# Performance work log

Measured on AMD Instinct MI355X. Metric: run time of the kernel, lower is better.

The kernel has to match this reference:

```python
import jax, jax.numpy as jnp
import numpy as np

N_NODES = 10000

def rgcn_layer(x, edge_index, basis, comp, root, bias):
    # x: [N, Fin]; edge_index: [R, 2, E] int; basis: [B, Fin, Fout]; comp: [R, B]
    R, _, E = edge_index.shape
    N = x.shape[0]
    src = edge_index[:, 0]  # [R, E]
    dst = edge_index[:, 1]  # [R, E]
    # basis-decomposed per-relation weights: W_r = sum_b comp[r,b] * basis[b]
    W = jnp.einsum('rb,bio->rio', comp, basis)          # [R, Fin, Fout]
    x_src = x[src]                                       # [R, E, Fin] gather
    msg = jnp.einsum('rei,rio->reo', x_src, W)           # [R, E, Fout]
    # per-relation mean aggregation onto destination nodes
    seg = (jnp.arange(R, dtype=dst.dtype)[:, None] * N + dst).reshape(-1)  # [R*E]
    agg = jax.ops.segment_sum(msg.reshape(R * E, -1), seg, num_segments=R * N)
    deg = jax.ops.segment_sum(jnp.ones((R * E,), x.dtype), seg, num_segments=R * N)
    agg = agg / jnp.maximum(deg, 1.0)[:, None]
    agg = agg.reshape(R, N, -1).sum(0)                   # sum over relations
    return agg + x @ root + bias


def setup_inputs() -> dict:
    key = jax.random.key(0)
    ks = jax.random.split(key, 10)
    s = 0.05  # scale params for numerical sanity
    return {
        'x_drug': jax.random.normal(ks[0], (N_NODES, 2048), jnp.float32),
        'drug_w': jax.random.normal(ks[1], (2048, 128), jnp.float32) * s,
        'edge_index': jax.random.randint(ks[2], (100, 2, 5000), 0, N_NODES, jnp.int32),
        'basis1': jax.random.normal(ks[3], (8, 128, 64), jnp.float32) * s,
        'comp1': jax.random.normal(ks[4], (100, 8), jnp.float32) * s,
        'root1': jax.random.normal(ks[5], (128, 64), jnp.float32) * s,
        'bias1': jnp.zeros((64,), jnp.float32),
        'basis2': jax.random.normal(ks[6], (8, 64, 20), jnp.float32) * s,
        'comp2': jax.random.normal(ks[7], (100, 8), jnp.float32) * s,
        'root2': jax.random.normal(ks[8], (64, 20), jnp.float32) * s,
        'bias2': jnp.zeros((20,), jnp.float32),
    }


def reference(x_drug, drug_w, edge_index, basis1, comp1, root1, bias1,
              basis2, comp2, root2, bias2):
    x = x_drug @ drug_w                                   # dense projection [N, 128]
    h = rgcn_layer(x, edge_index, basis1, comp1, root1, bias1)   # [N, 64]
    h = jax.nn.relu(h)
    out = rgcn_layer(h, edge_index, basis2, comp2, root2, bias2)  # [N, 20]
    return out
```

## Files before the change

kernel.cpp:

```cpp
#include <hip/hip_runtime.h>

#define NN 10000
#define RR 100
#define EE 5000
#define D0 2048
#define D1 128
#define D2 64
#define D3 20
#define NE (RR*EE)
#define MAXD 128

using short8  = __attribute__((ext_vector_type(8))) short;
using float4e = __attribute__((ext_vector_type(4))) float;

typedef const __attribute__((address_space(1))) void g_void;
typedef __attribute__((address_space(3))) void l_void;

__device__ __forceinline__ unsigned short f2bf(float f) {
  unsigned int u = __float_as_uint(f);
  unsigned int r = u + 0x7fffu + ((u >> 16) & 1u);
  return (unsigned short)(r >> 16);
}
__device__ __forceinline__ float bf2f(unsigned short u) {
  return __uint_as_float(((unsigned int)u) << 16);
}
__device__ __forceinline__ unsigned int pk2(float lo, float hi) {
  return ((unsigned int)f2bf(hi) << 16) | (unsigned int)f2bf(lo);
}

#define CURB 10
#define WTBLK 1024
#define W1BLK 288
#define W2BLK 72
__global__ __launch_bounds__(256) void prep_kernel(
    const float* __restrict__ W, const float* __restrict__ root1,
    const float* __restrict__ basis1, const float* __restrict__ root2,
    const float* __restrict__ basis2, int4* __restrict__ cur4,
    unsigned short* __restrict__ Btw, unsigned short* __restrict__ Wc1T,
    unsigned short* __restrict__ Wc2T) {
  const int b = blockIdx.x, tid = threadIdx.x;
  if (b < CURB) {
    int i = b * 256 + tid;
    if (i < 2504) cur4[i] = make_int4(0, 0, 0, 0);
  } else if (b < CURB + WTBLK) {
    int idx = (b - CURB) * 256 + tid;
    int n = idx >> 11, k = idx & 2047;
    Btw[idx] = f2bf(W[(size_t)k * 128 + n]);
  } else if (b < CURB + WTBLK + W1BLK) {
    int idx = (b - CURB - WTBLK) * 256 + tid;
    int o = idx / 1152, j = idx - o * 1152;
    float v = (j < 128) ? root1[j * 64 + o] : basis1[(j - 128) * 64 + o];
    Wc1T[idx] = f2bf(v);
  } else {
    int idx = (b - CURB - WTBLK - W1BLK) * 256 + tid;
    int c = idx / 576, j = idx - c * 576;
    float v = 0.f;
    if (c < 20) v = (j < 64) ? root2[j * 20 + c] : basis2[(j - 64) * 20 + c];
    Wc2T[idx] = f2bf(v);
  }
}

__global__ void scatter_kernel(const int* __restrict__ ei,
                               int* __restrict__ cur, int* __restrict__ rec) {
  int gid = blockIdx.x * 256 + threadIdx.x;
  if (gid >= NE) return;
  int r = gid / EE, e = gid - r * EE;
  int s = ei[r * 2 * EE + e];
  int d = ei[r * 2 * EE + EE + e];
  int p = atomicAdd(&cur[d], 1);
  if (p < MAXD) rec[d * MAXD + p] = (r << 14) | s;
}

__global__ __launch_bounds__(256) void finalize_kernel(
    const int* __restrict__ cur, const int* __restrict__ rec,
    float* __restrict__ esc) {
  __shared__ int hist[4][RR];
  const int tid = threadIdx.x;
  const int wv = tid >> 6, lane = tid & 63;
  const int n = blockIdx.x * 4 + wv;
  for (int i = lane; i < RR; i += 64) hist[wv][i] = 0;
  __syncthreads();
  int cnt = cur[n]; if (cnt > MAXD) cnt = MAXD;
  int r0 = 0, r1 = 0;
  if (lane < cnt) {
    r0 = rec[n * MAXD + lane] >> 14;
    atomicAdd(&hist[wv][r0], 1);
  }
  if (lane + 64 < cnt) {
    r1 = rec[n * MAXD + lane + 64] >> 14;
    atomicAdd(&hist[wv][r1], 1);
  }
  __syncthreads();
  if (lane < cnt)      esc[n * MAXD + lane]      = 1.0f / (float)hist[wv][r0];
  if (lane + 64 < cnt) esc[n * MAXD + lane + 64] = 1.0f / (float)hist[wv][r1];
}

__global__ __launch_bounds__(256) void gemm0_mfma(
    const float* __restrict__ A, const unsigned short* __restrict__ Btw,
    unsigned short* __restrict__ xb) {
  __shared__ __align__(16) unsigned short Asb[2][16 * 64];
  __shared__ __align__(16) unsigned short Bsb[2][128 * 64];
  const int tid = threadIdx.x;
  const int m0 = blockIdx.x * 16;
  const int wv = tid >> 6, lane = tid & 63;
  const int lrow = lane & 15, quad = lane >> 4;

  const int ar = tid >> 4, ag = tid & 15;
  const float* Ap = &A[(size_t)(m0 + ar) * D0 + ag * 4];
  const int aw = (ar * 128 + ((ag * 8) ^ ((ar & 7) << 4))) >> 1;

  const int rowB = wv * 32 + (lane >> 3);
  const int gch  = (lane & 7) ^ (lane >> 3);
  const unsigned short* BgBase = &Btw[(size_t)rowB * D0 + gch * 8];
  const int ldsB = wv * 2048;

  float4 a0;

#define G0_LOADB(buf, c)                                                     \
  { _Pragma("unroll")                                                        \
    for (int i = 0; i < 4; i++) {                                            \
      __builtin_amdgcn_global_load_lds(                                      \
          (g_void*)(BgBase + (size_t)i * 8 * D0 + (c) * 64),                 \
          (l_void*)&Bsb[buf][ldsB + i * 512], 16, 0, 0);                     \
    } }

#define G0_LOADA(c)  { a0 = *(const float4*)(Ap + (c) * 64); }

#define G0_STOREA(buf)                                                  \
  { uint2 p0;                                                           \
    p0.x = pk2(a0.x, a0.y); p0.y = pk2(a0.z, a0.w);                     \
    *(uint2*)&Asb[buf][aw] = p0; }

#define G0_COMPUTE(buf)                                                 \
  { const int aswz = (lrow & 7) << 4;                                   \
    _Pragma("unroll")                                                   \
    for (int kk = 0; kk < 2; kk++) {                                    \
      short8 af = *(const short8*)&Asb[buf][(lrow * 128 + ((quad * 16 + kk * 64) ^ aswz)) >> 1]; \
      _Pragma("unroll")                                                 \
      for (int nt = 0; nt < 2; nt++) {                                  \
        const int brow = wv * 32 + nt * 16 + lrow;                      \
        short8 bfr = *(const short8*)&Bsb[buf][(brow * 128 + ((quad * 16 + kk * 64) ^ ((brow & 7) << 4))) >> 1]; \
        acc[nt] = __builtin_amdgcn_mfma_f32_16x16x32_bf16(af, bfr, acc[nt], 0, 0, 0); \
      }                                                                 \
    } }

  float4e acc[2];
#pragma unroll
  for (int i = 0; i < 2; i++) { acc[i][0]=0.f; acc[i][1]=0.f; acc[i][2]=0.f; acc[i][3]=0.f; }

  G0_LOADB(0, 0);
  G0_LOADA(0);
  G0_STOREA(0);
  __syncthreads();

#pragma unroll 4
  for (int c = 0; c < 32; c++) {
    if (c < 31) {
      G0_LOADB((c + 1) & 1, c + 1);
      G0_LOADA(c + 1);
      __builtin_amdgcn_sched_barrier(0);
    }
    G0_COMPUTE(c & 1);
    if (c < 31) G0_STOREA((c + 1) & 1);
    __syncthreads();
  }

#pragma unroll
  for (int nt = 0; nt < 2; nt++) {
    const int col = wv * 32 + nt * 16 + lrow;
#pragma unroll
    for (int r = 0; r < 4; r++) {
      const int row = m0 + quad * 4 + r;
      xb[(size_t)row * D1 + col] = f2bf(acc[nt][r]);
    }
  }
}

__global__ __launch_bounds__(256) void agg1e_kernel(
    const unsigned short* __restrict__ xb, const int* __restrict__ cur,
    const int* __restrict__ rec, const float* __restrict__ esc,
    const float* __restrict__ comp, unsigned short* __restrict__ A1b) {
  __shared__ float s_comp[RR * 8];
  const int tid = threadIdx.x;
  for (int i = tid; i < RR * 8; i += 256) s_comp[i] = comp[i];
  __syncthreads();
  const int wv = tid >> 6, lane = tid & 63;
  const int n = blockIdx.x * 4 + wv;
  if (n >= NN) return;
  float acc[8][2];
#pragma unroll
  for (int b = 0; b < 8; b++) { acc[b][0] = 0.f; acc[b][1] = 0.f; }
  int cnt = cur[n]; if (cnt > MAXD) cnt = MAXD;
  const int beg = n * MAXD, end = beg + cnt;
  int idx = beg;
  for (; idx + 3 < end; idx += 4) {
    int rc[4]; float sc[4]; unsigned int xv[4];
#pragma unroll
    for (int u = 0; u < 4; u++) {
      rc[u] = rec[idx + u];
      sc[u] = esc[idx + u];
    }
#pragma unroll
    for (int u = 0; u < 4; u++)
      xv[u] = *(const unsigned int*)&xb[(size_t)(rc[u] & 16383) * D1 + lane * 2];
#pragma unroll
    for (int u = 0; u < 4; u++) {
      const float* cb = &s_comp[(rc[u] >> 14) * 8];
      float x0 = __uint_as_float((xv[u] & 0xffffu) << 16);
      float x1 = __uint_as_float(xv[u] & 0xffff0000u);
#pragma unroll
      for (int b = 0; b < 8; b++) {
        float w = sc[u] * cb[b];
        acc[b][0] += w * x0;
        acc[b][1] += w * x1;
      }
    }
  }
  for (; idx < end; idx++) {
    int rc = rec[idx];
    float sc = esc[idx];
    unsigned int xv = *(const unsigned int*)&xb[(size_t)(rc & 16383) * D1 + lane * 2];
    const float* cb = &s_comp[(rc >> 14) * 8];
    float x0 = __uint_as_float((xv & 0xffffu) << 16);
    float x1 = __uint_as_float(xv & 0xffff0000u);
#pragma unroll
    for (int b = 0; b < 8; b++) {
      float w = sc * cb[b];
      acc[b][0] += w * x0;
      acc[b][1] += w * x1;
    }
  }
#pragma unroll
  for (int b = 0; b < 8; b++) {
    ushort2 o; o.x = f2bf(acc[b][0]); o.y = f2bf(acc[b][1]);
    *(ushort2*)&A1b[(size_t)n * 1024 + b * 128 + lane * 2] = o;
  }
}

__global__ __launch_bounds__(256) void agg2e_kernel(
    const unsigned short* __restrict__ hb, const int* __restrict__ cur,
    const int* __restrict__ rec, const float* __restrict__ esc,
    const float* __restrict__ comp, unsigned short* __restrict__ A2b) {
  __shared__ float s_comp[RR * 8];
  const int tid = threadIdx.x;
  for (int i = tid; i < RR * 8; i += 256) s_comp[i] = comp[i];
  __syncthreads();
  const int wv = tid >> 6, lane = tid & 63;
  const int n = blockIdx.x * 4 + wv;
  if (n >= NN) return;
  float acc[8];
#pragma unroll
  for (int b = 0; b < 8; b++) acc[b] = 0.f;
  int cnt = cur[n]; if (cnt > MAXD) cnt = MAXD;
  const int beg = n * MAXD, end = beg + cnt;
  int idx = beg;
  for (; idx + 3 < end; idx += 4) {
    int rc[4]; float sc[4]; float hv[4];
#pragma unroll
    for (int u = 0; u < 4; u++) {
      rc[u] = rec[idx + u];
      sc[u] = esc[idx + u];
    }
#pragma unroll
    for (int u = 0; u < 4; u++)
      hv[u] = bf2f(hb[(size_t)(rc[u] & 16383) * D2 + lane]);
#pragma unroll
    for (int u = 0; u < 4; u++) {
      const float* cb = &s_comp[(rc[u] >> 14) * 8];
#pragma unroll
      for (int b = 0; b < 8; b++) acc[b] += sc[u] * cb[b] * hv[u];
    }
  }
  for (; idx < end; idx++) {
    int rc = rec[idx];
    float sc = esc[idx];
    float hv = bf2f(hb[(size_t)(rc & 16383) * D2 + lane]);
    const float* cb = &s_comp[(rc >> 14) * 8];
#pragma unroll
    for (int b = 0; b < 8; b++) acc[b] += sc * cb[b] * hv;
  }
#pragma unroll
  for (int b = 0; b < 8; b++)
    A2b[(size_t)n * 512 + b * 64 + lane] = f2bf(acc[b]);
}

__global__ __launch_bounds__(256) void hlayer_mfma(
    const unsigned short* __restrict__ xb, const unsigned short* __restrict__ A1b,
    const unsigned short* __restrict__ Wt, const float* __restrict__ bias1,
    unsigned short* __restrict__ hb) {
  __shared__ __align__(16) unsigned short Asb[2][32 * 64];
  __shared__ __align__(16) unsigned short Bsb[2][64 * 64];
  const int tid = threadIdx.x;
  const int m0 = blockIdx.x * 32;
  const int wv = tid >> 6, lane = tid & 63;
  const int lrow = lane & 15, quad = lane >> 4;
  const int mt = wv >> 1, nb = wv & 1;

  const int ar = tid >> 3, ac = tid & 7;
  int gr = m0 + ar; if (gr >= NN) gr = NN - 1;
  const unsigned short* Ax = &xb[(size_t)gr * D1 + ac * 8];
  const unsigned short* Aa = &A1b[(size_t)gr * 1024 + ac * 8];
  const int asw = (ar & 7) << 4;
  const int aw = (ar * 128 + ((ac * 16) ^ asw)) >> 1;

  const int br = tid >> 2, bq = tid & 3;
  const unsigned short* Bp = &Wt[(size_t)br * 1152 + bq * 16];
  const int bsw = (br & 7) << 4;
  const int bw0 = (br * 128 + ((bq * 32) ^ bsw)) >> 1;
  const int bw1 = (br * 128 + ((bq * 32 + 16) ^ bsw)) >> 1;

  uint4 ra, rb0, rb1;

#define H_LOADG(c)                                                       \
  { int kb = (c) * 64;                                                   \
    ra  = (kb < 128) ? *(const uint4*)(Ax + kb)                          \
                     : *(const uint4*)(Aa + (kb - 128));                 \
    rb0 = *(const uint4*)(Bp + kb);                                      \
    rb1 = *(const uint4*)(Bp + kb + 8); }

#define H_STOREL(buf)                                                    \
  { *(uint4*)&Asb[buf][aw]  = ra;                                        \
    *(uint4*)&Bsb[buf][bw0] = rb0;                                       \
    *(uint4*)&Bsb[buf][bw1] = rb1; }

#define H_COMPUTE(buf)                                                   \
  { const int arow = mt * 16 + lrow;                                     \
    const int aswz = (arow & 7) << 4;                                    \
    _Pragma("unroll")                                                    \
    for (int kk = 0; kk < 2; kk++) {                                     \
      short8 af = *(const short8*)&Asb[buf][(arow * 128 + ((quad * 16 + kk * 64) ^ aswz)) >> 1]; \
      _Pragma("unroll")                                                  \
      for (int nt = 0; nt < 2; nt++) {                                   \
        const int brow = nb * 32 + nt * 16 + lrow;                       \
        short8 bfr = *(const short8*)&Bsb[buf][(brow * 128 + ((quad * 16 + kk * 64) ^ ((brow & 7) << 4))) >> 1]; \
        acc[nt] = __builtin_amdgcn_mfma_f32_16x16x32_bf16(af, bfr, acc[nt], 0, 0, 0); \
      }                                                                  \
    } }

  float4e acc[2];
#pragma unroll
  for (int i = 0; i < 2; i++) { acc[i][0]=0.f; acc[i][1]=0.f; acc[i][2]=0.f; acc[i][3]=0.f; }

  H_LOADG(0);
  H_STOREL(0);
  __syncthreads();

#pragma unroll
  for (int c = 0; c < 18; c++) {
    if (c < 17) {
      H_LOADG(c + 1);
      __builtin_amdgcn_sched_barrier(0);
    }
    H_COMPUTE(c & 1);
    if (c < 17) H_STOREL((c + 1) & 1);
    __syncthreads();
  }

#pragma unroll
  for (int nt = 0; nt < 2; nt++) {
    int col = nb * 32 + nt * 16 + lrow;
    float bv = bias1[col];
#pragma unroll
    for (int r = 0; r < 4; r++) {
      int row = m0 + mt * 16 + quad * 4 + r;
      if (row < NN)
        hb[(size_t)row * D2 + col] = f2bf(fmaxf(acc[nt][r] + bv, 0.f));
    }
  }
}

__global__ __launch_bounds__(256) void out_mfma(
    const unsigned short* __restrict__ hb, const unsigned short* __restrict__ A2b,
    const unsigned short* __restrict__ Wt, const float* __restrict__ bias2,
    float* __restrict__ out) {
  __shared__ __align__(16) unsigned short Asb[2][32 * 64];
  __shared__ __align__(16) unsigned short Bsb[2][32 * 64];
  const int tid = threadIdx.x;
  const int m0 = blockIdx.x * 32;
  const int wv = tid >> 6, lane = tid & 63;
  const int lrow = lane & 15, quad = lane >> 4;
  const int mt = wv >> 1, ntn = wv & 1;

  const int ar = tid >> 3, ac = tid & 7;
  int gr = m0 + ar; if (gr >= NN) gr = NN - 1;
  const unsigned short* Ah = &hb[(size_t)gr * D2 + ac * 8];
  const unsigned short* Aa = &A2b[(size_t)gr * 512 + ac * 8];
  const unsigned short* Bp = &Wt[(size_t)ar * 576 + ac * 8];
  const int asw = (ar & 7) << 4;
  const int aw = (ar * 128 + ((ac * 16) ^ asw)) >> 1;

  uint4 ra, rb;

#define O_LOADG(c)                                                       \
  { int kb = (c) * 64;                                                   \
    ra = (kb < 64) ? *(const uint4*)(Ah)                                 \
                   : *(const uint4*)(Aa + (kb - 64));                    \
    rb = *(const uint4*)(Bp + kb); }

#define O_STOREL(buf)                                                    \
  { *(uint4*)&Asb[buf][aw] = ra;                                         \
    *(uint4*)&Bsb[buf][aw] = rb; }

#define O_COMPUTE(buf)                                                   \
  { const int arow = mt * 16 + lrow;                                     \
    const int aswz = (arow & 7) << 4;                                    \
    const int brow = ntn * 16 + lrow;                                    \
    const int bswz = (brow & 7) << 4;                                    \
    _Pragma("unroll")                                                    \
    for (int kk = 0; kk < 2; kk++) {                                     \
      short8 af = *(const short8*)&Asb[buf][(arow * 128 + ((quad * 16 + kk * 64) ^ aswz)) >> 1]; \
      short8 bfr = *(const short8*)&Bsb[buf][(brow * 128 + ((quad * 16 + kk * 64) ^ bswz)) >> 1]; \
      acc = __builtin_amdgcn_mfma_f32_16x16x32_bf16(af, bfr, acc, 0, 0, 0); \
    } }

  float4e acc;
  acc[0]=0.f; acc[1]=0.f; acc[2]=0.f; acc[3]=0.f;

  O_LOADG(0);
  O_STOREL(0);
  __syncthreads();

#pragma unroll
  for (int c = 0; c < 9; c++) {
    if (c < 8) {
      O_LOADG(c + 1);
      __builtin_amdgcn_sched_barrier(0);
    }
    O_COMPUTE(c & 1);
    if (c < 8) O_STOREL((c + 1) & 1);
    __syncthreads();
  }

  int col = ntn * 16 + lrow;
  if (col < D3) {
    float bv = bias2[col];
#pragma unroll
    for (int r = 0; r < 4; r++) {
      int row = m0 + mt * 16 + quad * 4 + r;
      if (row < NN)
        out[(size_t)row * D3 + col] = acc[r] + bv;
    }
  }
}

extern "C" void kernel_launch(void* const* d_in, const int* in_sizes, int n_in,
                              void* d_out, int out_size, void* d_ws,
                              size_t ws_size, hipStream_t stream) {
  const float* x_drug = (const float*)d_in[0];
  const float* drug_w = (const float*)d_in[1];
  const int*   ei     = (const int*)d_in[2];
  const float* basis1 = (const float*)d_in[3];
  const float* comp1  = (const float*)d_in[4];
  const float* root1  = (const float*)d_in[5];
  const float* bias1  = (const float*)d_in[6];
  const float* basis2 = (const float*)d_in[7];
  const float* comp2  = (const float*)d_in[8];
  const float* root2  = (const float*)d_in[9];
  const float* bias2  = (const float*)d_in[10];
  float* out = (float*)d_out;

  float* ws = (float*)d_ws;
  int*   cur  = (int*)ws;
  int*   rec  = cur + 10016;
  float* esc  = (float*)(rec + NN * MAXD);
  unsigned short* xb   = (unsigned short*)(esc + NN * MAXD);
  unsigned short* hb   = (unsigned short*)((float*)xb + 640000);
  unsigned short* Btw  = (unsigned short*)((float*)hb + 320000);
  unsigned short* Wc1T = (unsigned short*)((float*)Btw + 131072);
  unsigned short* Wc2T = (unsigned short*)((float*)Wc1T + 36864);
  float* R1 = (float*)Wc2T + 9216;
  unsigned short* A1b = (unsigned short*)R1;
  unsigned short* A2b = (unsigned short*)R1;

  prep_kernel<<<CURB + WTBLK + W1BLK + W2BLK, 256, 0, stream>>>(
      drug_w, root1, basis1, root2, basis2, (int4*)cur, Btw, Wc1T, Wc2T);

  scatter_kernel<<<(NE + 255) / 256, 256, 0, stream>>>(ei, cur, rec);
  finalize_kernel<<<NN / 4, 256, 0, stream>>>(cur, rec, esc);

  gemm0_mfma<<<NN / 16, 256, 0, stream>>>(x_drug, Btw, xb);

  agg1e_kernel<<<(NN + 3) / 4, 256, 0, stream>>>(xb, cur, rec, esc, comp1, A1b);
  hlayer_mfma<<<(NN + 31) / 32, 256, 0, stream>>>(xb, A1b, Wc1T, bias1, hb);

  agg2e_kernel<<<(NN + 3) / 4, 256, 0, stream>>>(hb, cur, rec, esc, comp2, A2b);
  out_mfma<<<(NN + 31) / 32, 256, 0, stream>>>(hb, A2b, Wc2T, bias2, out);
}
```

Before: 152.0 us.

## Fuse degree normalization into aggregation kernels and triple-buffer gemm0 B tiles

Drops the separate finalize kernel and its per-edge scale array. Each aggregation kernel now builds a per-node relation histogram in shared memory and looks up reciprocal degrees there, which removes one launch and the global esc reads and writes. The histogram work is repeated in both aggregation kernels. The input GEMM moves to a three-stage B buffer with two register A stages and explicit vmcnt waits so loads run two tiles ahead, at the cost of more LDS per block.

```diff
diff --git a/kernel.cpp b/kernel.cpp
--- a/kernel.cpp
+++ b/kernel.cpp
@@ -71,35 +71,11 @@
   if (p < MAXD) rec[d * MAXD + p] = (r << 14) | s;
 }
 
-__global__ __launch_bounds__(256) void finalize_kernel(
-    const int* __restrict__ cur, const int* __restrict__ rec,
-    float* __restrict__ esc) {
-  __shared__ int hist[4][RR];
-  const int tid = threadIdx.x;
-  const int wv = tid >> 6, lane = tid & 63;
-  const int n = blockIdx.x * 4 + wv;
-  for (int i = lane; i < RR; i += 64) hist[wv][i] = 0;
-  __syncthreads();
-  int cnt = cur[n]; if (cnt > MAXD) cnt = MAXD;
-  int r0 = 0, r1 = 0;
-  if (lane < cnt) {
-    r0 = rec[n * MAXD + lane] >> 14;
-    atomicAdd(&hist[wv][r0], 1);
-  }
-  if (lane + 64 < cnt) {
-    r1 = rec[n * MAXD + lane + 64] >> 14;
-    atomicAdd(&hist[wv][r1], 1);
-  }
-  __syncthreads();
-  if (lane < cnt)      esc[n * MAXD + lane]      = 1.0f / (float)hist[wv][r0];
-  if (lane + 64 < cnt) esc[n * MAXD + lane + 64] = 1.0f / (float)hist[wv][r1];
-}
-
-__global__ __launch_bounds__(256) void gemm0_mfma(
+__global__ __launch_bounds__(256, 3) void gemm0_mfma(
     const float* __restrict__ A, const unsigned short* __restrict__ Btw,
     unsigned short* __restrict__ xb) {
   __shared__ __align__(16) unsigned short Asb[2][16 * 64];
-  __shared__ __align__(16) unsigned short Bsb[2][128 * 64];
+  __shared__ __align__(16) unsigned short Bsb[3][128 * 64];
   const int tid = threadIdx.x;
   const int m0 = blockIdx.x * 16;
   const int wv = tid >> 6, lane = tid & 63;
@@ -114,7 +90,7 @@
   const unsigned short* BgBase = &Btw[(size_t)rowB * D0 + gch * 8];
   const int ldsB = wv * 2048;
 
-  float4 a0;
+  float4 a0, a1;
 
 #define G0_LOADB(buf, c)                                                     \
   { _Pragma("unroll")                                                        \
@@ -124,22 +100,22 @@
           (l_void*)&Bsb[buf][ldsB + i * 512], 16, 0, 0);                     \
     } }
 
-#define G0_LOADA(c)  { a0 = *(const float4*)(Ap + (c) * 64); }
-
-#define G0_STOREA(buf)                                                  \
+#define G0_LOADA(reg, c)  { reg = *(const float4*)(Ap + (c) * 64); }
+
+#define G0_PACKA(reg, buf)                                              \
   { uint2 p0;                                                           \
-    p0.x = pk2(a0.x, a0.y); p0.y = pk2(a0.z, a0.w);                     \
+    p0.x = pk2(reg.x, reg.y); p0.y = pk2(reg.z, reg.w);                 \
     *(uint2*)&Asb[buf][aw] = p0; }
 
-#define G0_COMPUTE(buf)                                                 \
+#define G0_COMPUTE(abuf, bbuf)                                          \
   { const int aswz = (lrow & 7) << 4;                                   \
     _Pragma("unroll")                                                   \
     for (int kk = 0; kk < 2; kk++) {                                    \
-      short8 af = *(const short8*)&Asb[buf][(lrow * 128 + ((quad * 16 + kk * 64) ^ aswz)) >> 1]; \
+      short8 af = *(const short8*)&Asb[abuf][(lrow * 128 + ((quad * 16 + kk * 64) ^ aswz)) >> 1]; \
       _Pragma("unroll")                                                 \
       for (int nt = 0; nt < 2; nt++) {                                  \
         const int brow = wv * 32 + nt * 16 + lrow;                      \
-        short8 bfr = *(const short8*)&Bsb[buf][(brow * 128 + ((quad * 16 + kk * 64) ^ ((brow & 7) << 4))) >> 1]; \
+        short8 bfr = *(const short8*)&Bsb[bbuf][(brow * 128 + ((quad * 16 + kk * 64) ^ ((brow & 7) << 4))) >> 1]; \
         acc[nt] = __builtin_amdgcn_mfma_f32_16x16x32_bf16(af, bfr, acc[nt], 0, 0, 0); \
       }                                                                 \
     } }
@@ -148,21 +124,27 @@
 #pragma unroll
   for (int i = 0; i < 2; i++) { acc[i][0]=0.f; acc[i][1]=0.f; acc[i][2]=0.f; acc[i][3]=0.f; }
 
+  G0_LOADA(a0, 0);
   G0_LOADB(0, 0);
-  G0_LOADA(0);
-  G0_STOREA(0);
-  __syncthreads();
-
-#pragma unroll 4
+  G0_LOADB(1, 1);
+  G0_PACKA(a0, 0);
+  G0_LOADA(a1, 1);
+  asm volatile("s_waitcnt vmcnt(5) lgkmcnt(0)\ns_barrier" ::: "memory");
+
+#pragma unroll
   for (int c = 0; c < 32; c++) {
-    if (c < 31) {
-      G0_LOADB((c + 1) & 1, c + 1);
-      G0_LOADA(c + 1);
+    if (c <= 29) {
+      G0_LOADB((c + 2) % 3, c + 2);
+      if ((c & 1) == 0) { G0_LOADA(a0, c + 2); }
+      else              { G0_LOADA(a1, c + 2); }
       __builtin_amdgcn_sched_barrier(0);
     }
-    G0_COMPUTE(c & 1);
-    if (c < 31) G0_STOREA((c + 1) & 1);
-    __syncthreads();
+    G0_COMPUTE(c & 1, c % 3);
+    if (c <= 30) {
+      if (((c + 1) & 1) == 0) { G0_PACKA(a0, 0); }
+      else                    { G0_PACKA(a1, 1); }
+      asm volatile("s_waitcnt vmcnt(5) lgkmcnt(0)\ns_barrier" ::: "memory");
+    }
   }
 
 #pragma unroll
@@ -178,28 +160,38 @@
 
 __global__ __launch_bounds__(256) void agg1e_kernel(
     const unsigned short* __restrict__ xb, const int* __restrict__ cur,
-    const int* __restrict__ rec, const float* __restrict__ esc,
-    const float* __restrict__ comp, unsigned short* __restrict__ A1b) {
+    const int* __restrict__ rec, const float* __restrict__ comp,
+    unsigned short* __restrict__ A1b) {
   __shared__ float s_comp[RR * 8];
+  __shared__ float s_rcp[4][RR];
   const int tid = threadIdx.x;
   for (int i = tid; i < RR * 8; i += 256) s_comp[i] = comp[i];
-  __syncthreads();
   const int wv = tid >> 6, lane = tid & 63;
   const int n = blockIdx.x * 4 + wv;
-  if (n >= NN) return;
+  int* hist = (int*)&s_rcp[wv][0];
+  for (int i = lane; i < RR; i += 64) hist[i] = 0;
+  __syncthreads();
+  int cnt = cur[n]; if (cnt > MAXD) cnt = MAXD;
+  if (lane < cnt)      atomicAdd(&hist[rec[n * MAXD + lane] >> 14], 1);
+  if (lane + 64 < cnt) atomicAdd(&hist[rec[n * MAXD + lane + 64] >> 14], 1);
+  __syncthreads();
+  for (int i = lane; i < RR; i += 64) {
+    int h = hist[i];
+    s_rcp[wv][i] = 1.0f / (float)h;
+  }
+  __syncthreads();
+
   float acc[8][2];
 #pragma unroll
   for (int b = 0; b < 8; b++) { acc[b][0] = 0.f; acc[b][1] = 0.f; }
-  int cnt = cur[n]; if (cnt > MAXD) cnt = MAXD;
   const int beg = n * MAXD, end = beg + cnt;
   int idx = beg;
   for (; idx + 3 < end; idx += 4) {
     int rc[4]; float sc[4]; unsigned int xv[4];
 #pragma unroll
-    for (int u = 0; u < 4; u++) {
-      rc[u] = rec[idx + u];
-      sc[u] = esc[idx + u];
-    }
+    for (int u = 0; u < 4; u++) rc[u] = rec[idx + u];
+#pragma unroll
+    for (int u = 0; u < 4; u++) sc[u] = s_rcp[wv][rc[u] >> 14];
 #pragma unroll
     for (int u = 0; u < 4; u++)
       xv[u] = *(const unsigned int*)&xb[(size_t)(rc[u] & 16383) * D1 + lane * 2];
@@ -218,7 +210,7 @@
   }
   for (; idx < end; idx++) {
     int rc = rec[idx];
-    float sc = esc[idx];
+    float sc = s_rcp[wv][rc >> 14];
     unsigned int xv = *(const unsigned int*)&xb[(size_t)(rc & 16383) * D1 + lane * 2];
     const float* cb = &s_comp[(rc >> 14) * 8];
     float x0 = __uint_as_float((xv & 0xffffu) << 16);
@@ -239,28 +231,38 @@
 
 __global__ __launch_bounds__(256) void agg2e_kernel(
     const unsigned short* __restrict__ hb, const int* __restrict__ cur,
-    const int* __restrict__ rec, const float* __restrict__ esc,
-    const float* __restrict__ comp, unsigned short* __restrict__ A2b) {
+    const int* __restrict__ rec, const float* __restrict__ comp,
+    unsigned short* __restrict__ A2b) {
   __shared__ float s_comp[RR * 8];
+  __shared__ float s_rcp[4][RR];
   const int tid = threadIdx.x;
   for (int i = tid; i < RR * 8; i += 256) s_comp[i] = comp[i];
-  __syncthreads();
   const int wv = tid >> 6, lane = tid & 63;
   const int n = blockIdx.x * 4 + wv;
-  if (n >= NN) return;
+  int* hist = (int*)&s_rcp[wv][0];
+  for (int i = lane; i < RR; i += 64) hist[i] = 0;
+  __syncthreads();
+  int cnt = cur[n]; if (cnt > MAXD) cnt = MAXD;
+  if (lane < cnt)      atomicAdd(&hist[rec[n * MAXD + lane] >> 14], 1);
+  if (lane + 64 < cnt) atomicAdd(&hist[rec[n * MAXD + lane + 64] >> 14], 1);
+  __syncthreads();
+  for (int i = lane; i < RR; i += 64) {
+    int h = hist[i];
+    s_rcp[wv][i] = 1.0f / (float)h;
+  }
+  __syncthreads();
+
   float acc[8];
 #pragma unroll
   for (int b = 0; b < 8; b++) acc[b] = 0.f;
-  int cnt = cur[n]; if (cnt > MAXD) cnt = MAXD;
   const int beg = n * MAXD, end = beg + cnt;
   int idx = beg;
   for (; idx + 3 < end; idx += 4) {
     int rc[4]; float sc[4]; float hv[4];
 #pragma unroll
-    for (int u = 0; u < 4; u++) {
-      rc[u] = rec[idx + u];
-      sc[u] = esc[idx + u];
-    }
+    for (int u = 0; u < 4; u++) rc[u] = rec[idx + u];
+#pragma unroll
+    for (int u = 0; u < 4; u++) sc[u] = s_rcp[wv][rc[u] >> 14];
 #pragma unroll
     for (int u = 0; u < 4; u++)
       hv[u] = bf2f(hb[(size_t)(rc[u] & 16383) * D2 + lane]);
@@ -273,7 +275,7 @@
   }
   for (; idx < end; idx++) {
     int rc = rec[idx];
-    float sc = esc[idx];
+    float sc = s_rcp[wv][rc >> 14];
     float hv = bf2f(hb[(size_t)(rc & 16383) * D2 + lane]);
     const float* cb = &s_comp[(rc >> 14) * 8];
 #pragma unroll
@@ -462,8 +464,7 @@
   float* ws = (float*)d_ws;
   int*   cur  = (int*)ws;
   int*   rec  = cur + 10016;
-  float* esc  = (float*)(rec + NN * MAXD);
-  unsigned short* xb   = (unsigned short*)(esc + NN * MAXD);
+  unsigned short* xb   = (unsigned short*)(rec + NN * MAXD);
   unsigned short* hb   = (unsigned short*)((float*)xb + 640000);
   unsigned short* Btw  = (unsigned short*)((float*)hb + 320000);
   unsigned short* Wc1T = (unsigned short*)((float*)Btw + 131072);
@@ -476,13 +477,12 @@
       drug_w, root1, basis1, root2, basis2, (int4*)cur, Btw, Wc1T, Wc2T);
 
   scatter_kernel<<<(NE + 255) / 256, 256, 0, stream>>>(ei, cur, rec);
-  finalize_kernel<<<NN / 4, 256, 0, stream>>>(cur, rec, esc);
 
   gemm0_mfma<<<NN / 16, 256, 0, stream>>>(x_drug, Btw, xb);
 
-  agg1e_kernel<<<(NN + 3) / 4, 256, 0, stream>>>(xb, cur, rec, esc, comp1, A1b);
+  agg1e_kernel<<<NN / 4, 256, 0, stream>>>(xb, cur, rec, comp1, A1b);
   hlayer_mfma<<<(NN + 31) / 32, 256, 0, stream>>>(xb, A1b, Wc1T, bias1, hb);
 
-  agg2e_kernel<<<(NN + 3) / 4, 256, 0, stream>>>(hb, cur, rec, esc, comp2, A2b);
+  agg2e_kernel<<<NN / 4, 256, 0, stream>>>(hb, cur, rec, comp2, A2b);
   out_mfma<<<(NN + 31) / 32, 256, 0, stream>>>(hb, A2b, Wc2T, bias2, out);
 }
```

New measurement: 147.6 us. 2.9% less time.
